# Kernel tuning notes

Hardware: AMD Instinct MI355X
Metric: run time of the kernel (lower is better)

Reference implementation:

```python
import jax, jax.numpy as jnp
import numpy as np

N = 100_000       # SUBJECT nodes
E = 1_000_000     # edges per relation
R = 3             # number of metapath relations
DIM_IN = 128
DIM_H = 128
HEADS = 8
D = DIM_H // HEADS   # per-head dim = 16
DIM_OUT = 4


def setup_inputs() -> dict:
    key = jax.random.key(0)
    ks = jax.random.split(key, 16)
    x = jax.random.normal(ks[0], (N, DIM_IN), dtype=jnp.float32)
    ei = [jax.random.randint(ks[1 + r], (2, E), 0, N, dtype=jnp.int32) for r in range(R)]
    s = 0.05
    return {
        "x": x,
        "edge_index_r0": ei[0],
        "edge_index_r1": ei[1],
        "edge_index_r2": ei[2],
        "proj_w": jax.random.normal(ks[4], (DIM_H, DIM_IN), dtype=jnp.float32) * s,
        "proj_b": jnp.zeros((DIM_H,), dtype=jnp.float32),
        "att_src": jax.random.normal(ks[5], (R, HEADS, D), dtype=jnp.float32) * s,
        "att_dst": jax.random.normal(ks[6], (R, HEADS, D), dtype=jnp.float32) * s,
        "k_w": jax.random.normal(ks[7], (DIM_H, DIM_H), dtype=jnp.float32) * s,
        "k_b": jnp.zeros((DIM_H,), dtype=jnp.float32),
        "q": jax.random.normal(ks[8], (DIM_H,), dtype=jnp.float32) * s,
        "lin_w": jax.random.normal(ks[9], (DIM_OUT, DIM_H), dtype=jnp.float32) * s,
        "lin_b": jnp.zeros((DIM_OUT,), dtype=jnp.float32),
    }


def _relation_out(h, a_src, a_dst, row, col, n):
    # GAT-style edge attention with softmax over destination neighborhoods.
    alpha = jax.nn.leaky_relu(a_src[row] + a_dst[col], 0.2)          # [E, H]
    m = jax.ops.segment_max(alpha, col, num_segments=n)              # [N, H]
    m = jax.lax.stop_gradient(jnp.where(jnp.isfinite(m), m, 0.0))
    e = jnp.exp(alpha - m[col])
    denom = jax.ops.segment_sum(e, col, num_segments=n)              # [N, H]
    alpha = e / (denom[col] + 1e-16)                                 # [E, H]
    msg = h[row] * alpha[..., None]                                  # [E, H, D]
    agg = jax.ops.segment_sum(msg, col, num_segments=n)              # [N, H, D]
    return jax.nn.relu(agg).reshape(n, HEADS * D)                    # [N, F]


def reference(x, edge_index_r0, edge_index_r1, edge_index_r2,
              proj_w, proj_b, att_src, att_dst, k_w, k_b, q, lin_w, lin_b):
    n = x.shape[0]
    h = (x @ proj_w.T + proj_b).reshape(n, HEADS, D)                 # node-type projection
    # per-node attention logits for every relation: [R, N, H]
    a_src = jnp.einsum('nhd,rhd->rnh', h, att_src)
    a_dst = jnp.einsum('nhd,rhd->rnh', h, att_dst)
    edge_indices = [edge_index_r0, edge_index_r1, edge_index_r2]
    outs = [_relation_out(h, a_src[r], a_dst[r], edge_indices[r][0], edge_indices[r][1], n)
            for r in range(R)]
    outs = jnp.stack(outs)                                           # [R, N, F]
    # semantic-level attention over metapaths
    score = jnp.einsum('f,rf->r', q, jnp.tanh(outs @ k_w.T + k_b).mean(axis=1))
    attn = jax.nn.softmax(score)                                     # [R]
    fused = jnp.einsum('r,rnf->nf', attn, outs)                      # [N, F]
    return fused @ lin_w.T + lin_b                                   # [N, DIM_OUT]
```

## Files before the change

kernel.cpp:

```cpp
#include <hip/hip_runtime.h>

#define N_NODES 100000
#define E_EDGES 1000000
#define R_REL   3
#define NBATCH  6250
#define NBLK    391
#define SEMBLK  782
#define CNT_BLKS  11721
#define PROJ_BLKS 391
#define A_BLKS    3125
#define BSUM_BLKS 1173
#define FILL_BLKS 3907
#define PULL_BLKS 3125

using bf16x8 = __attribute__((ext_vector_type(8))) short;
using f32x4  = __attribute__((ext_vector_type(4))) float;
using u32x2  = __attribute__((ext_vector_type(2))) unsigned int;

__device__ __forceinline__ float lrelu(float x) { return fmaxf(x, 0.2f * x); }

__device__ __forceinline__ short f2bf(float f) {
    unsigned u = __builtin_bit_cast(unsigned, f);
    u += 0x7FFFu + ((u >> 16) & 1u);
    return (short)(u >> 16);
}
__device__ __forceinline__ float bf_lo(unsigned u) {
    return __builtin_bit_cast(float, u << 16);
}
__device__ __forceinline__ float bf_hi(unsigned u) {
    return __builtin_bit_cast(float, u & 0xFFFF0000u);
}
__device__ __forceinline__ float bf2f(unsigned short u) {
    return __builtin_bit_cast(float, ((unsigned)u) << 16);
}

__global__ __launch_bounds__(256) void prep_kernel(
    const float* __restrict__ kw, const float* __restrict__ pw,
    const float* __restrict__ lw,
    short* __restrict__ kwB, short* __restrict__ pwB, short* __restrict__ linB)
{
    int idx = blockIdx.x * 256 + threadIdx.x;
    int which, rem;
    if      (idx < 16384) { which = 0; rem = idx; }
    else if (idx < 32768) { which = 1; rem = idx - 16384; }
    else if (idx < 34816) { which = 2; rem = idx - 32768; }
    else return;
    int e = rem & 7, lane = (rem >> 3) & 63, t = rem >> 9;
    int tj = (which == 2) ? 0 : (t >> 2);
    int tk = (which == 2) ? t : (t & 3);
    int j = tj * 16 + (lane & 15);
    int k = tk * 32 + (lane >> 4) * 8 + e;
    const float* src = (which == 0) ? kw : (which == 1) ? pw : lw;
    float v = (which == 2 && j >= 4) ? 0.f : src[j * 128 + k];
    short* dst = (which == 0) ? kwB : (which == 1) ? pwB : linB;
    dst[rem] = f2bf(v);
}

__device__ __forceinline__ void proj_body(
    int bx, const float* __restrict__ x, const short* __restrict__ pwB,
    const float* __restrict__ pb, unsigned short* __restrict__ h_bf)
{
    int wave = threadIdx.x >> 6, lane = threadIdx.x & 63;
    int row16 = lane & 15, kq = lane >> 4;
    for (int b = bx * 4 + wave; b < NBATCH; b += PROJ_BLKS * 4) {
        int nbase = b * 16;
        bf16x8 A[4];
        #pragma unroll
        for (int tk = 0; tk < 4; ++tk) {
            const float* px = x + (size_t)(nbase + row16) * 128 + tk * 32 + kq * 8;
            f32x4 lo = *(const f32x4*)px;
            f32x4 hi = *(const f32x4*)(px + 4);
            bf16x8 a;
            a[0] = f2bf(lo[0]); a[1] = f2bf(lo[1]); a[2] = f2bf(lo[2]); a[3] = f2bf(lo[3]);
            a[4] = f2bf(hi[0]); a[5] = f2bf(hi[1]); a[6] = f2bf(hi[2]); a[7] = f2bf(hi[3]);
            A[tk] = a;
        }
        #pragma unroll
        for (int tj = 0; tj < 8; ++tj) {
            f32x4 c = {0.f, 0.f, 0.f, 0.f};
            #pragma unroll
            for (int tk = 0; tk < 4; ++tk) {
                bf16x8 B = *(const bf16x8*)(pwB + ((size_t)(tj * 4 + tk) * 64 + lane) * 8);
                c = __builtin_amdgcn_mfma_f32_16x16x32_bf16(A[tk], B, c, 0, 0, 0);
            }
            int j = tj * 16 + row16;
            float bias = pb[j];
            #pragma unroll
            for (int m = 0; m < 4; ++m) {
                int n = nbase + kq * 4 + m;
                h_bf[(size_t)n * 128 + j] = (unsigned short)f2bf(c[m] + bias);
            }
        }
    }
}

__global__ __launch_bounds__(256) void count_proj_kernel(
    const int* __restrict__ e0, const int* __restrict__ e1, const int* __restrict__ e2,
    int* __restrict__ cnt, int* __restrict__ rank,
    const float* __restrict__ x, const short* __restrict__ pwB,
    const float* __restrict__ pb, unsigned short* __restrict__ h_bf)
{
    int b = blockIdx.x;
    if (b < CNT_BLKS) {
        int r = b / 3907, eb = b % 3907;
        const int* ei = (r == 0) ? e0 : (r == 1) ? e1 : e2;
        int e = eb * 256 + threadIdx.x;
        if (e < E_EDGES) {
            int k = atomicAdd(&cnt[r * N_NODES + ei[E_EDGES + e]], 1);
            rank[(size_t)r * E_EDGES + e] = k;
        }
    } else {
        proj_body(b - CNT_BLKS, x, pwB, pb, h_bf);
    }
}

__global__ __launch_bounds__(256) void a_bsum_kernel(
    const unsigned short* __restrict__ h_bf, const float* __restrict__ att_src,
    const float* __restrict__ att_dst,
    float* __restrict__ a_src, float* __restrict__ a_dst,
    const int* __restrict__ cnt, int* __restrict__ bsums)
{
    int b = blockIdx.x;
    if (b < A_BLKS) {
        int idx = b * 256 + threadIdx.x;
        if (idx >= N_NODES * 8) return;
        int n = idx >> 3, hd = idx & 7;
        float hv[16];
        const unsigned short* ph = h_bf + (size_t)n * 128 + hd * 16;
        #pragma unroll
        for (int d = 0; d < 16; ++d) hv[d] = bf2f(ph[d]);
        #pragma unroll
        for (int r = 0; r < 3; ++r) {
            float vs = 0.f, vd = 0.f;
            #pragma unroll
            for (int d = 0; d < 16; ++d) {
                vs += hv[d] * att_src[(r * 8 + hd) * 16 + d];
                vd += hv[d] * att_dst[(r * 8 + hd) * 16 + d];
            }
            a_src[((size_t)r * N_NODES + n) * 8 + hd] = vs;
            a_dst[((size_t)r * N_NODES + n) * 8 + hd] = vd;
        }
    } else {
        __shared__ int sh[256];
        int bb = b - A_BLKS;
        int r = bb / NBLK, blk = bb % NBLK, t = threadIdx.x;
        int i = blk * 256 + t;
        sh[t] = (i < N_NODES) ? cnt[r * N_NODES + i] : 0;
        __syncthreads();
        for (int d = 128; d > 0; d >>= 1) {
            if (t < d) sh[t] += sh[t + d];
            __syncthreads();
        }
        if (t == 0) bsums[r * NBLK + blk] = sh[0];
    }
}

__global__ __launch_bounds__(512) void bscan_kernel(
    const int* __restrict__ bsums, int* __restrict__ bpre)
{
    __shared__ int sh[512];
    int r = blockIdx.x, t = threadIdx.x;
    sh[t] = (t < NBLK) ? bsums[r * NBLK + t] : 0;
    __syncthreads();
    for (int d = 1; d < 512; d <<= 1) {
        int v = (t >= d) ? sh[t - d] : 0;
        __syncthreads();
        sh[t] += v;
        __syncthreads();
    }
    if (t < NBLK) bpre[r * NBLK + t] = (t > 0) ? sh[t - 1] : 0;
}

__global__ __launch_bounds__(256) void offwrite_kernel(
    const int* __restrict__ cnt, const int* __restrict__ bpre,
    int* __restrict__ off)
{
    __shared__ int sh[256];
    int r = blockIdx.y, b = blockIdx.x, t = threadIdx.x;
    int i = b * 256 + t;
    int c = (i < N_NODES) ? cnt[r * N_NODES + i] : 0;
    sh[t] = c;
    __syncthreads();
    for (int d = 1; d < 256; d <<= 1) {
        int v = (t >= d) ? sh[t - d] : 0;
        __syncthreads();
        sh[t] += v;
        __syncthreads();
    }
    if (i < N_NODES)
        off[r * N_NODES + i] = r * E_EDGES + bpre[r * NBLK + b] + (sh[t] - c);
}

__device__ __forceinline__ void fill_body(
    int r, int eb,
    const int* __restrict__ e0, const int* __restrict__ e1, const int* __restrict__ e2,
    const int* __restrict__ off, const int* __restrict__ rank,
    int* __restrict__ csr_rows)
{
    const int* ei = (r == 0) ? e0 : (r == 1) ? e1 : e2;
    int e = eb * 256 + threadIdx.x;
    if (e >= E_EDGES) return;
    int col = ei[E_EDGES + e];
    int pos = off[r * N_NODES + col] + rank[(size_t)r * E_EDGES + e];
    csr_rows[pos] = ei[e];
}

__global__ __launch_bounds__(256) void fill_kernel(
    const int* __restrict__ e0, const int* __restrict__ e1, const int* __restrict__ e2,
    const int* __restrict__ off, const int* __restrict__ rank,
    int* __restrict__ csr_rows, int r)
{
    fill_body(r, blockIdx.x, e0, e1, e2, off, rank, csr_rows);
}

__device__ __forceinline__ void pull_body(
    int bx, int r,
    const unsigned short* __restrict__ h_bf, const float* __restrict__ a_src,
    const float* __restrict__ a_dst, const int* __restrict__ cnt,
    const int* __restrict__ off, const int* __restrict__ csr_rows,
    unsigned int* __restrict__ outs_bf)
{
    int tid = threadIdx.x;
    int wave = tid >> 6, lane = tid & 63;
    int half = lane >> 5, hl = lane & 31;
    int hd = hl >> 2;
    const size_t rbase = (size_t)r * N_NODES;
    const int CSR_LAST = R_REL * E_EDGES - 1;

    int nb = (bx * 8 + wave * 2 + half) * 4;

    int deg4[4], dm1[4], st4[4];
    float adv[4];
    int kmax = 0;
    #pragma unroll
    for (int i = 0; i < 4; ++i) {
        size_t rn = rbase + (nb + i);
        deg4[i] = cnt[rn];
        st4[i]  = off[rn];
        dm1[i]  = max(deg4[i] - 1, 0);
        adv[i]  = a_dst[rn * 8 + hd];
        kmax = max(kmax, deg4[i]);
    }
    float acc[4][4] = {};
    float den[4] = {0.f, 0.f, 0.f, 0.f};

    for (int k = 0; k < kmax; k += 2) {
        int rowA[4], rowB[4];
        #pragma unroll
        for (int i = 0; i < 4; ++i) {
            int kA = min(k, dm1[i]), kB = min(k + 1, dm1[i]);
            rowA[i] = csr_rows[min(st4[i] + kA, CSR_LAST)];
            rowB[i] = csr_rows[min(st4[i] + kB, CSR_LAST)];
        }
        float aA[4], aB[4];
        u32x2 hA[4], hB[4];
        #pragma unroll
        for (int i = 0; i < 4; ++i) {
            aA[i] = a_src[(rbase + rowA[i]) * 8 + hd];
            aB[i] = a_src[(rbase + rowB[i]) * 8 + hd];
            hA[i] = *(const u32x2*)(h_bf + (size_t)rowA[i] * 128 + 4 * hl);
            hB[i] = *(const u32x2*)(h_bf + (size_t)rowB[i] * 128 + 4 * hl);
        }
        #pragma unroll
        for (int i = 0; i < 4; ++i) {
            float eA = __expf(lrelu(aA[i] + adv[i]));
            float eB = __expf(lrelu(aB[i] + adv[i]));
            eA = (k     < deg4[i]) ? eA : 0.f;
            eB = (k + 1 < deg4[i]) ? eB : 0.f;
            acc[i][0] += eA * bf_lo(hA[i][0]);
            acc[i][1] += eA * bf_hi(hA[i][0]);
            acc[i][2] += eA * bf_lo(hA[i][1]);
            acc[i][3] += eA * bf_hi(hA[i][1]);
            den[i]    += eA;
            acc[i][0] += eB * bf_lo(hB[i][0]);
            acc[i][1] += eB * bf_hi(hB[i][0]);
            acc[i][2] += eB * bf_lo(hB[i][1]);
            acc[i][3] += eB * bf_hi(hB[i][1]);
            den[i]    += eB;
        }
    }
    #pragma unroll
    for (int i = 0; i < 4; ++i) {
        float inv = 1.f / (den[i] + 1e-16f);
        float o0 = fmaxf(acc[i][0] * inv, 0.f);
        float o1 = fmaxf(acc[i][1] * inv, 0.f);
        float o2 = fmaxf(acc[i][2] * inv, 0.f);
        float o3 = fmaxf(acc[i][3] * inv, 0.f);
        u32x2 p;
        p[0] = (unsigned)(unsigned short)f2bf(o0) | ((unsigned)(unsigned short)f2bf(o1) << 16);
        p[1] = (unsigned)(unsigned short)f2bf(o2) | ((unsigned)(unsigned short)f2bf(o3) << 16);
        *(u32x2*)(outs_bf + (size_t)(nb + i) * 64 + 2 * hl) = p;
    }
}

__global__ __launch_bounds__(256) void pull_kernel(
    const unsigned short* __restrict__ h_bf, const float* __restrict__ a_src,
    const float* __restrict__ a_dst, const int* __restrict__ cnt,
    const int* __restrict__ off, const int* __restrict__ csr_rows,
    unsigned int* __restrict__ outs_bf, int r)
{
    pull_body(blockIdx.x, r, h_bf, a_src, a_dst, cnt, off, csr_rows, outs_bf);
}

__global__ __launch_bounds__(256) void pull0_fill12_kernel(
    const unsigned short* __restrict__ h_bf, const float* __restrict__ a_src,
    const float* __restrict__ a_dst, const int* __restrict__ cnt,
    const int* __restrict__ off, const int* __restrict__ csr_rows,
    unsigned int* __restrict__ outs_bf,
    const int* __restrict__ e0, const int* __restrict__ e1, const int* __restrict__ e2,
    const int* __restrict__ rank, int* __restrict__ csr_w)
{
    int b = blockIdx.x;
    if (b < PULL_BLKS) {
        pull_body(b, 0, h_bf, a_src, a_dst, cnt, off, csr_rows, outs_bf);
    } else {
        int bb = b - PULL_BLKS;
        int r = 1 + bb / FILL_BLKS, eb = bb % FILL_BLKS;
        fill_body(r, eb, e0, e1, e2, off, rank, csr_w);
    }
}

__global__ __launch_bounds__(256) void semantic_kernel(
    const unsigned short* __restrict__ outs_bf,
    const short* __restrict__ kwB, const short* __restrict__ linB,
    const float* __restrict__ kb,
    float* __restrict__ proj_out, float* __restrict__ redpart, int r)
{
    __shared__ float sh[4][128];
    int wave = threadIdx.x >> 6, lane = threadIdx.x & 63;
    int row16 = lane & 15, kq = lane >> 4;
    const size_t rbase = (size_t)r * N_NODES;

    float kbv[8];
    #pragma unroll
    for (int tj = 0; tj < 8; ++tj) kbv[tj] = kb[tj * 16 + row16];
    float red_acc[8] = {0.f,0.f,0.f,0.f,0.f,0.f,0.f,0.f};

    for (int b = blockIdx.x * 4 + wave; b < NBATCH; b += gridDim.x * 4) {
        int nbase = b * 16;
        bf16x8 A[4];
        #pragma unroll
        for (int tk = 0; tk < 4; ++tk)
            A[tk] = *(const bf16x8*)(outs_bf + (size_t)(nbase + row16) * 128 + tk * 32 + kq * 8);

        #pragma unroll
        for (int tj = 0; tj < 8; ++tj) {
            f32x4 c = {0.f, 0.f, 0.f, 0.f};
            #pragma unroll
            for (int tk = 0; tk < 4; ++tk) {
                bf16x8 B = *(const bf16x8*)(kwB + ((size_t)(tj * 4 + tk) * 64 + lane) * 8);
                c = __builtin_amdgcn_mfma_f32_16x16x32_bf16(A[tk], B, c, 0, 0, 0);
            }
            float ts = 0.f;
            #pragma unroll
            for (int m = 0; m < 4; ++m) {
                float s = c[m] + kbv[tj];
                float ex = __expf(2.f * s);
                ts += 1.f - 2.f / (ex + 1.f);
            }
            red_acc[tj] += ts;
        }
        {
            f32x4 c = {0.f, 0.f, 0.f, 0.f};
            #pragma unroll
            for (int tk = 0; tk < 4; ++tk) {
                bf16x8 B = *(const bf16x8*)(linB + ((size_t)tk * 64 + lane) * 8);
                c = __builtin_amdgcn_mfma_f32_16x16x32_bf16(A[tk], B, c, 0, 0, 0);
            }
            if (row16 < 4) {
                #pragma unroll
                for (int m = 0; m < 4; ++m) {
                    int n = nbase + kq * 4 + m;
                    proj_out[(rbase + n) * 4 + row16] = c[m];
                }
            }
        }
    }

    #pragma unroll
    for (int tj = 0; tj < 8; ++tj) {
        float v = red_acc[tj];
        v += __shfl_xor(v, 16);
        v += __shfl_xor(v, 32);
        if (lane < 16) sh[wave][tj * 16 + lane] = v;
    }
    __syncthreads();
    int t = threadIdx.x;
    if (t < 128) {
        float p = sh[0][t] + sh[1][t] + sh[2][t] + sh[3][t];
        redpart[((size_t)r * SEMBLK + blockIdx.x) * 128 + t] = p;
    }
}

__global__ __launch_bounds__(256) void redreduce_kernel(
    const float* __restrict__ redpart, float* __restrict__ red)
{
    __shared__ float sh[2][128];
    int r = blockIdx.x;
    int t = threadIdx.x;
    int j = t & 127, half = t >> 7;
    float s = 0.f;
    for (int b = half; b < SEMBLK; b += 2)
        s += redpart[((size_t)r * SEMBLK + b) * 128 + j];
    sh[half][j] = s;
    __syncthreads();
    if (t < 128) red[r * 128 + t] = sh[0][t] + sh[1][t];
}

__global__ void attn_kernel(const float* __restrict__ red, const float* __restrict__ q,
                            float* __restrict__ attn)
{
    int lane = threadIdx.x;
    float p[3];
    #pragma unroll
    for (int r = 0; r < 3; ++r) {
        float v = q[lane] * red[r * 128 + lane] + q[lane + 64] * red[r * 128 + lane + 64];
        for (int sft = 32; sft; sft >>= 1) v += __shfl_down(v, sft);
        p[r] = v;
    }
    if (lane == 0) {
        float s0 = p[0] / (float)N_NODES;
        float s1 = p[1] / (float)N_NODES;
        float s2 = p[2] / (float)N_NODES;
        float m = fmaxf(s0, fmaxf(s1, s2));
        float e0 = __expf(s0 - m), e1 = __expf(s1 - m), e2 = __expf(s2 - m);
        float inv = 1.f / (e0 + e1 + e2);
        attn[0] = e0 * inv; attn[1] = e1 * inv; attn[2] = e2 * inv;
    }
}

__global__ __launch_bounds__(256) void final_kernel(
    const float* __restrict__ proj_out, const float* __restrict__ attn,
    const float* __restrict__ lb, float* __restrict__ out)
{
    int i = blockIdx.x * 256 + threadIdx.x;
    if (i >= N_NODES * 4) return;
    int o = i & 3;
    out[i] = attn[0] * proj_out[i]
           + attn[1] * proj_out[(size_t)N_NODES * 4 + i]
           + attn[2] * proj_out[(size_t)2 * N_NODES * 4 + i]
           + lb[o];
}

extern "C" void kernel_launch(void* const* d_in, const int* in_sizes, int n_in,
                              void* d_out, int out_size, void* d_ws, size_t ws_size,
                              hipStream_t stream)
{
    const float* x       = (const float*)d_in[0];
    const int*   e0      = (const int*)d_in[1];
    const int*   e1      = (const int*)d_in[2];
    const int*   e2      = (const int*)d_in[3];
    const float* pw      = (const float*)d_in[4];
    const float* pb      = (const float*)d_in[5];
    const float* att_src = (const float*)d_in[6];
    const float* att_dst = (const float*)d_in[7];
    const float* kw      = (const float*)d_in[8];
    const float* kb      = (const float*)d_in[9];
    const float* q       = (const float*)d_in[10];
    const float* lw      = (const float*)d_in[11];
    const float* lb      = (const float*)d_in[12];
    float* out = (float*)d_out;

    float* ws = (float*)d_ws;
    unsigned short* h_bf    = (unsigned short*)ws;
    float*          a_src   = ws + 6400000;
    float*          a_dst   = ws + 8800000;
    unsigned int*   outs_bf = (unsigned int*)(ws + 11200000);
    float*          proj_out= ws + 17600000;
    float*          red     = ws + 18800000;
    float*          attn    = ws + 18800384;
    short*          kwB     = (short*)(ws + 18800388);
    short*          pwB     = (short*)(ws + 18808580);
    short*          linB    = (short*)(ws + 18816772);
    int*            cnt     = (int*)(ws + 18817796);
    int*            off     = (int*)(ws + 19117796);
    int*            csr_rows= (int*)(ws + 19417796);
    int*            bsums   = (int*)(ws + 22417796);
    int*            bpre    = (int*)(ws + 22418969);
    float*          redpart = ws + 22420224;

    const size_t BIG_NEED = (size_t)(22720512 + 3000000) * 4;
    bool big = ws_size >= BIG_NEED;
    int* rank = big ? (int*)(ws + 22720512)
                    : (int*)outs_bf;

    hipMemsetAsync(cnt, 0, 300000 * sizeof(int), stream);

    prep_kernel<<<dim3(136), dim3(256), 0, stream>>>(kw, pw, lw, kwB, pwB, linB);
    count_proj_kernel<<<dim3(CNT_BLKS + PROJ_BLKS), dim3(256), 0, stream>>>(
        e0, e1, e2, cnt, rank, x, pwB, pb, h_bf);
    a_bsum_kernel<<<dim3(A_BLKS + BSUM_BLKS), dim3(256), 0, stream>>>(
        h_bf, att_src, att_dst, a_src, a_dst, cnt, bsums);
    bscan_kernel<<<dim3(3), dim3(512), 0, stream>>>(bsums, bpre);
    offwrite_kernel<<<dim3(NBLK, 3), dim3(256), 0, stream>>>(cnt, bpre, off);

    if (big) {
        fill_kernel<<<dim3(FILL_BLKS), dim3(256), 0, stream>>>(
            e0, e1, e2, off, rank, csr_rows, 0);
        pull0_fill12_kernel<<<dim3(PULL_BLKS + 2 * FILL_BLKS), dim3(256), 0, stream>>>(
            h_bf, a_src, a_dst, cnt, off, csr_rows, outs_bf,
            e0, e1, e2, rank, csr_rows);
        semantic_kernel<<<dim3(SEMBLK), dim3(256), 0, stream>>>(
            (const unsigned short*)outs_bf, kwB, linB, kb, proj_out, redpart, 0);
        for (int r = 1; r < 3; ++r) {
            pull_kernel<<<dim3(PULL_BLKS), dim3(256), 0, stream>>>(
                h_bf, a_src, a_dst, cnt, off, csr_rows, outs_bf, r);
            semantic_kernel<<<dim3(SEMBLK), dim3(256), 0, stream>>>(
                (const unsigned short*)outs_bf, kwB, linB, kb, proj_out, redpart, r);
        }
    } else {
        for (int r = 0; r < 3; ++r)
            fill_kernel<<<dim3(FILL_BLKS), dim3(256), 0, stream>>>(
                e0, e1, e2, off, rank, csr_rows, r);
        for (int r = 0; r < 3; ++r) {
            pull_kernel<<<dim3(PULL_BLKS), dim3(256), 0, stream>>>(
                h_bf, a_src, a_dst, cnt, off, csr_rows, outs_bf, r);
            semantic_kernel<<<dim3(SEMBLK), dim3(256), 0, stream>>>(
                (const unsigned short*)outs_bf, kwB, linB, kb, proj_out, redpart, r);
        }
    }

    redreduce_kernel<<<dim3(3), dim3(256), 0, stream>>>(redpart, red);
    attn_kernel<<<dim3(1), dim3(64), 0, stream>>>(red, q, attn);
    final_kernel<<<dim3(1563), dim3(256), 0, stream>>>(proj_out, attn, lb, out);
}
```

Measured before the change: 532.0 us.

## Double-buffer relation outputs and co-schedule pull with semantic, move attention logits into fill

Adds a second bf16 output buffer so the pull for relation r+1 and the semantic projection for relation r run in one fused launch. The per-node attention logit computation moves out of the bsum kernel and into the fill kernel for relation 0, and bsum becomes a standalone 2D-grid kernel. It also sets unroll 1 on the MFMA tj loops and adds occupancy hints of 6 blocks to reduce register pressure. The aim is to overlap the gather-bound pull with the MFMA-bound semantic work and cut launch boundaries, at the cost of more workspace and a path that only activates when the larger workspace is available.

Result: slower. 567.9 us (+6.7%).

```diff
diff --git a/kernel.cpp b/kernel.cpp
--- a/kernel.cpp
+++ b/kernel.cpp
@@ -9,7 +9,6 @@
 #define CNT_BLKS  11721
 #define PROJ_BLKS 391
 #define A_BLKS    3125
-#define BSUM_BLKS 1173
 #define FILL_BLKS 3907
 #define PULL_BLKS 3125
 
@@ -75,7 +74,7 @@
             a[4] = f2bf(hi[0]); a[5] = f2bf(hi[1]); a[6] = f2bf(hi[2]); a[7] = f2bf(hi[3]);
             A[tk] = a;
         }
-        #pragma unroll
+        #pragma unroll 1
         for (int tj = 0; tj < 8; ++tj) {
             f32x4 c = {0.f, 0.f, 0.f, 0.f};
             #pragma unroll
@@ -94,7 +93,7 @@
     }
 }
 
-__global__ __launch_bounds__(256) void count_proj_kernel(
+__global__ __launch_bounds__(256, 6) void count_proj_kernel(
     const int* __restrict__ e0, const int* __restrict__ e1, const int* __restrict__ e2,
     int* __restrict__ cnt, int* __restrict__ rank,
     const float* __restrict__ x, const short* __restrict__ pwB,
@@ -114,45 +113,19 @@
     }
 }
 
-__global__ __launch_bounds__(256) void a_bsum_kernel(
-    const unsigned short* __restrict__ h_bf, const float* __restrict__ att_src,
-    const float* __restrict__ att_dst,
-    float* __restrict__ a_src, float* __restrict__ a_dst,
+__global__ __launch_bounds__(256) void bsum_kernel(
     const int* __restrict__ cnt, int* __restrict__ bsums)
 {
-    int b = blockIdx.x;
-    if (b < A_BLKS) {
-        int idx = b * 256 + threadIdx.x;
-        if (idx >= N_NODES * 8) return;
-        int n = idx >> 3, hd = idx & 7;
-        float hv[16];
-        const unsigned short* ph = h_bf + (size_t)n * 128 + hd * 16;
-        #pragma unroll
-        for (int d = 0; d < 16; ++d) hv[d] = bf2f(ph[d]);
-        #pragma unroll
-        for (int r = 0; r < 3; ++r) {
-            float vs = 0.f, vd = 0.f;
-            #pragma unroll
-            for (int d = 0; d < 16; ++d) {
-                vs += hv[d] * att_src[(r * 8 + hd) * 16 + d];
-                vd += hv[d] * att_dst[(r * 8 + hd) * 16 + d];
-            }
-            a_src[((size_t)r * N_NODES + n) * 8 + hd] = vs;
-            a_dst[((size_t)r * N_NODES + n) * 8 + hd] = vd;
-        }
-    } else {
-        __shared__ int sh[256];
-        int bb = b - A_BLKS;
-        int r = bb / NBLK, blk = bb % NBLK, t = threadIdx.x;
-        int i = blk * 256 + t;
-        sh[t] = (i < N_NODES) ? cnt[r * N_NODES + i] : 0;
+    __shared__ int sh[256];
+    int r = blockIdx.y, b = blockIdx.x, t = threadIdx.x;
+    int i = b * 256 + t;
+    sh[t] = (i < N_NODES) ? cnt[r * N_NODES + i] : 0;
+    __syncthreads();
+    for (int d = 128; d > 0; d >>= 1) {
+        if (t < d) sh[t] += sh[t + d];
         __syncthreads();
-        for (int d = 128; d > 0; d >>= 1) {
-            if (t < d) sh[t] += sh[t + d];
-            __syncthreads();
-        }
-        if (t == 0) bsums[r * NBLK + blk] = sh[0];
-    }
+    }
+    if (t == 0) bsums[r * NBLK + b] = sh[0];
 }
 
 __global__ __launch_bounds__(512) void bscan_kernel(
@@ -191,6 +164,31 @@
         off[r * N_NODES + i] = r * E_EDGES + bpre[r * NBLK + b] + (sh[t] - c);
 }
 
+__device__ __forceinline__ void a_body(
+    int bx, const unsigned short* __restrict__ h_bf,
+    const float* __restrict__ att_src, const float* __restrict__ att_dst,
+    float* __restrict__ a_src, float* __restrict__ a_dst)
+{
+    int idx = bx * 256 + threadIdx.x;
+    if (idx >= N_NODES * 8) return;
+    int n = idx >> 3, hd = idx & 7;
+    float hv[16];
+    const unsigned short* ph = h_bf + (size_t)n * 128 + hd * 16;
+    #pragma unroll
+    for (int d = 0; d < 16; ++d) hv[d] = bf2f(ph[d]);
+    #pragma unroll
+    for (int r = 0; r < 3; ++r) {
+        float vs = 0.f, vd = 0.f;
+        #pragma unroll
+        for (int d = 0; d < 16; ++d) {
+            vs += hv[d] * att_src[(r * 8 + hd) * 16 + d];
+            vd += hv[d] * att_dst[(r * 8 + hd) * 16 + d];
+        }
+        a_src[((size_t)r * N_NODES + n) * 8 + hd] = vs;
+        a_dst[((size_t)r * N_NODES + n) * 8 + hd] = vd;
+    }
+}
+
 __device__ __forceinline__ void fill_body(
     int r, int eb,
     const int* __restrict__ e0, const int* __restrict__ e1, const int* __restrict__ e2,
@@ -205,12 +203,21 @@
     csr_rows[pos] = ei[e];
 }
 
-__global__ __launch_bounds__(256) void fill_kernel(
+__global__ __launch_bounds__(256) void a_fill_kernel(
+    const unsigned short* __restrict__ h_bf, const float* __restrict__ att_src,
+    const float* __restrict__ att_dst, float* __restrict__ a_src,
+    float* __restrict__ a_dst,
     const int* __restrict__ e0, const int* __restrict__ e1, const int* __restrict__ e2,
     const int* __restrict__ off, const int* __restrict__ rank,
-    int* __restrict__ csr_rows, int r)
-{
-    fill_body(r, blockIdx.x, e0, e1, e2, off, rank, csr_rows);
+    int* __restrict__ csr_rows)
+{
+    int b = blockIdx.x;
+    if (b < A_BLKS) {
+        a_body(b, h_bf, att_src, att_dst, a_src, a_dst);
+    } else {
+        int bb = b - A_BLKS;
+        fill_body(bb / FILL_BLKS, bb % FILL_BLKS, e0, e1, e2, off, rank, csr_rows);
+    }
 }
 
 __device__ __forceinline__ void pull_body(
@@ -293,35 +300,8 @@
     }
 }
 
-__global__ __launch_bounds__(256) void pull_kernel(
-    const unsigned short* __restrict__ h_bf, const float* __restrict__ a_src,
-    const float* __restrict__ a_dst, const int* __restrict__ cnt,
-    const int* __restrict__ off, const int* __restrict__ csr_rows,
-    unsigned int* __restrict__ outs_bf, int r)
-{
-    pull_body(blockIdx.x, r, h_bf, a_src, a_dst, cnt, off, csr_rows, outs_bf);
-}
-
-__global__ __launch_bounds__(256) void pull0_fill12_kernel(
-    const unsigned short* __restrict__ h_bf, const float* __restrict__ a_src,
-    const float* __restrict__ a_dst, const int* __restrict__ cnt,
-    const int* __restrict__ off, const int* __restrict__ csr_rows,
-    unsigned int* __restrict__ outs_bf,
-    const int* __restrict__ e0, const int* __restrict__ e1, const int* __restrict__ e2,
-    const int* __restrict__ rank, int* __restrict__ csr_w)
-{
-    int b = blockIdx.x;
-    if (b < PULL_BLKS) {
-        pull_body(b, 0, h_bf, a_src, a_dst, cnt, off, csr_rows, outs_bf);
-    } else {
-        int bb = b - PULL_BLKS;
-        int r = 1 + bb / FILL_BLKS, eb = bb % FILL_BLKS;
-        fill_body(r, eb, e0, e1, e2, off, rank, csr_w);
-    }
-}
-
-__global__ __launch_bounds__(256) void semantic_kernel(
-    const unsigned short* __restrict__ outs_bf,
+__device__ __forceinline__ void semantic_body(
+    int bx, const unsigned short* __restrict__ outs_bf,
     const short* __restrict__ kwB, const short* __restrict__ linB,
     const float* __restrict__ kb,
     float* __restrict__ proj_out, float* __restrict__ redpart, int r)
@@ -336,14 +316,14 @@
     for (int tj = 0; tj < 8; ++tj) kbv[tj] = kb[tj * 16 + row16];
     float red_acc[8] = {0.f,0.f,0.f,0.f,0.f,0.f,0.f,0.f};
 
-    for (int b = blockIdx.x * 4 + wave; b < NBATCH; b += gridDim.x * 4) {
+    for (int b = bx * 4 + wave; b < NBATCH; b += SEMBLK * 4) {
         int nbase = b * 16;
         bf16x8 A[4];
         #pragma unroll
         for (int tk = 0; tk < 4; ++tk)
             A[tk] = *(const bf16x8*)(outs_bf + (size_t)(nbase + row16) * 128 + tk * 32 + kq * 8);
 
-        #pragma unroll
+        #pragma unroll 1
         for (int tj = 0; tj < 8; ++tj) {
             f32x4 c = {0.f, 0.f, 0.f, 0.f};
             #pragma unroll
@@ -388,7 +368,59 @@
     int t = threadIdx.x;
     if (t < 128) {
         float p = sh[0][t] + sh[1][t] + sh[2][t] + sh[3][t];
-        redpart[((size_t)r * SEMBLK + blockIdx.x) * 128 + t] = p;
+        redpart[((size_t)r * SEMBLK + bx) * 128 + t] = p;
+    }
+}
+
+__global__ __launch_bounds__(256) void pull_kernel(
+    const unsigned short* __restrict__ h_bf, const float* __restrict__ a_src,
+    const float* __restrict__ a_dst, const int* __restrict__ cnt,
+    const int* __restrict__ off, const int* __restrict__ csr_rows,
+    unsigned int* __restrict__ outs_bf, int r)
+{
+    pull_body(blockIdx.x, r, h_bf, a_src, a_dst, cnt, off, csr_rows, outs_bf);
+}
+
+__global__ __launch_bounds__(256) void semantic_kernel(
+    const unsigned short* __restrict__ outs_bf,
+    const short* __restrict__ kwB, const short* __restrict__ linB,
+    const float* __restrict__ kb,
+    float* __restrict__ proj_out, float* __restrict__ redpart, int r)
+{
+    semantic_body(blockIdx.x, outs_bf, kwB, linB, kb, proj_out, redpart, r);
+}
+
+__global__ __launch_bounds__(256) void pull0_fill12_kernel(
+    const unsigned short* __restrict__ h_bf, const float* __restrict__ a_src,
+    const float* __restrict__ a_dst, const int* __restrict__ cnt,
+    const int* __restrict__ off, const int* __restrict__ csr_rows,
+    unsigned int* __restrict__ outs_bf,
+    const int* __restrict__ e0, const int* __restrict__ e1, const int* __restrict__ e2,
+    const int* __restrict__ rank, int* __restrict__ csr_w)
+{
+    int b = blockIdx.x;
+    if (b < PULL_BLKS) {
+        pull_body(b, 0, h_bf, a_src, a_dst, cnt, off, csr_rows, outs_bf);
+    } else {
+        int bb = b - PULL_BLKS;
+        fill_body(1 + bb / FILL_BLKS, bb % FILL_BLKS, e0, e1, e2, off, rank, csr_w);
+    }
+}
+
+__global__ __launch_bounds__(256, 6) void pull_sem_kernel(
+    const unsigned short* __restrict__ h_bf, const float* __restrict__ a_src,
+    const float* __restrict__ a_dst, const int* __restrict__ cnt,
+    const int* __restrict__ off, const int* __restrict__ csr_rows,
+    unsigned int* __restrict__ outsW, const unsigned short* __restrict__ outsR,
+    const short* __restrict__ kwB, const short* __restrict__ linB,
+    const float* __restrict__ kb, float* __restrict__ proj_out,
+    float* __restrict__ redpart, int rpull, int rsem)
+{
+    int b = blockIdx.x;
+    if (b < PULL_BLKS) {
+        pull_body(b, rpull, h_bf, a_src, a_dst, cnt, off, csr_rows, outsW);
+    } else {
+        semantic_body(b - PULL_BLKS, outsR, kwB, linB, kb, proj_out, redpart, rsem);
     }
 }
 
@@ -465,7 +497,7 @@
     unsigned short* h_bf    = (unsigned short*)ws;
     float*          a_src   = ws + 6400000;
     float*          a_dst   = ws + 8800000;
-    unsigned int*   outs_bf = (unsigned int*)(ws + 11200000);
+    unsigned int*   outs0   = (unsigned int*)(ws + 11200000);
     float*          proj_out= ws + 17600000;
     float*          red     = ws + 18800000;
     float*          attn    = ws + 18800384;
@@ -479,44 +511,58 @@
     int*            bpre    = (int*)(ws + 22418969);
     float*          redpart = ws + 22420224;
 
-    const size_t BIG_NEED = (size_t)(22720512 + 3000000) * 4;
-    bool big = ws_size >= BIG_NEED;
-    int* rank = big ? (int*)(ws + 22720512)
-                    : (int*)outs_bf;
+    const size_t P1_NEED = (size_t)(22720512 + 3000000) * 4;
+    const size_t P2_NEED = (size_t)(22720512 + 3000000 + 6400000) * 4;
+    bool p2 = ws_size >= P2_NEED;
+    bool p1 = ws_size >= P1_NEED;
+    int* rank = p1 ? (int*)(ws + 22720512) : (int*)outs0;
+    unsigned int* outs1 = p2 ? (unsigned int*)(ws + 25720512) : outs0;
 
     hipMemsetAsync(cnt, 0, 300000 * sizeof(int), stream);
 
     prep_kernel<<<dim3(136), dim3(256), 0, stream>>>(kw, pw, lw, kwB, pwB, linB);
     count_proj_kernel<<<dim3(CNT_BLKS + PROJ_BLKS), dim3(256), 0, stream>>>(
         e0, e1, e2, cnt, rank, x, pwB, pb, h_bf);
-    a_bsum_kernel<<<dim3(A_BLKS + BSUM_BLKS), dim3(256), 0, stream>>>(
-        h_bf, att_src, att_dst, a_src, a_dst, cnt, bsums);
+    bsum_kernel<<<dim3(NBLK, 3), dim3(256), 0, stream>>>(cnt, bsums);
     bscan_kernel<<<dim3(3), dim3(512), 0, stream>>>(bsums, bpre);
     offwrite_kernel<<<dim3(NBLK, 3), dim3(256), 0, stream>>>(cnt, bpre, off);
 
-    if (big) {
-        fill_kernel<<<dim3(FILL_BLKS), dim3(256), 0, stream>>>(
-            e0, e1, e2, off, rank, csr_rows, 0);
+    if (p2) {
+        a_fill_kernel<<<dim3(A_BLKS + FILL_BLKS), dim3(256), 0, stream>>>(
+            h_bf, att_src, att_dst, a_src, a_dst, e0, e1, e2, off, rank, csr_rows);
         pull0_fill12_kernel<<<dim3(PULL_BLKS + 2 * FILL_BLKS), dim3(256), 0, stream>>>(
-            h_bf, a_src, a_dst, cnt, off, csr_rows, outs_bf,
+            h_bf, a_src, a_dst, cnt, off, csr_rows, outs0,
+            e0, e1, e2, rank, csr_rows);
+        pull_sem_kernel<<<dim3(PULL_BLKS + SEMBLK), dim3(256), 0, stream>>>(
+            h_bf, a_src, a_dst, cnt, off, csr_rows, outs1,
+            (const unsigned short*)outs0, kwB, linB, kb, proj_out, redpart, 1, 0);
+        pull_sem_kernel<<<dim3(PULL_BLKS + SEMBLK), dim3(256), 0, stream>>>(
+            h_bf, a_src, a_dst, cnt, off, csr_rows, outs0,
+            (const unsigned short*)outs1, kwB, linB, kb, proj_out, redpart, 2, 1);
+        semantic_kernel<<<dim3(SEMBLK), dim3(256), 0, stream>>>(
+            (const unsigned short*)outs0, kwB, linB, kb, proj_out, redpart, 2);
+    } else if (p1) {
+        a_fill_kernel<<<dim3(A_BLKS + FILL_BLKS), dim3(256), 0, stream>>>(
+            h_bf, att_src, att_dst, a_src, a_dst, e0, e1, e2, off, rank, csr_rows);
+        pull0_fill12_kernel<<<dim3(PULL_BLKS + 2 * FILL_BLKS), dim3(256), 0, stream>>>(
+            h_bf, a_src, a_dst, cnt, off, csr_rows, outs0,
             e0, e1, e2, rank, csr_rows);
         semantic_kernel<<<dim3(SEMBLK), dim3(256), 0, stream>>>(
-            (const unsigned short*)outs_bf, kwB, linB, kb, proj_out, redpart, 0);
+            (const unsigned short*)outs0, kwB, linB, kb, proj_out, redpart, 0);
         for (int r = 1; r < 3; ++r) {
             pull_kernel<<<dim3(PULL_BLKS), dim3(256), 0, stream>>>(
-                h_bf, a_src, a_dst, cnt, off, csr_rows, outs_bf, r);
+                h_bf, a_src, a_dst, cnt, off, csr_rows, outs0, r);
             semantic_kernel<<<dim3(SEMBLK), dim3(256), 0, stream>>>(
-                (const unsigned short*)outs_bf, kwB, linB, kb, proj_out, redpart, r);
+                (const unsigned short*)outs0, kwB, linB, kb, proj_out, redpart, r);
         }
     } else {
-        for (int r = 0; r < 3; ++r)
-            fill_kernel<<<dim3(FILL_BLKS), dim3(256), 0, stream>>>(
-                e0, e1, e2, off, rank, csr_rows, r);
+        a_fill_kernel<<<dim3(A_BLKS + 3 * FILL_BLKS), dim3(256), 0, stream>>>(
+            h_bf, att_src, att_dst, a_src, a_dst, e0, e1, e2, off, rank, csr_rows);
         for (int r = 0; r < 3; ++r) {
             pull_kernel<<<dim3(PULL_BLKS), dim3(256), 0, stream>>>(
-                h_bf, a_src, a_dst, cnt, off, csr_rows, outs_bf, r);
+                h_bf, a_src, a_dst, cnt, off, csr_rows, outs0, r);
             semantic_kernel<<<dim3(SEMBLK), dim3(256), 0, stream>>>(
-                (const unsigned short*)outs_bf, kwB, linB, kb, proj_out, redpart, r);
+                (const unsigned short*)outs0, kwB, linB, kb, proj_out, redpart, r);
         }
     }
 
```

## Fuse semantic attention into pull kernel via LDS and regroup kernel launches

Applied to the files above, without the earlier changes.

The per-relation aggregation kernel now writes its bf16 outputs to shared memory and immediately runs the key-projection MFMA, tanh-sum and output projection within the same block, eliminating the global outs buffer and separate semantic kernels. The attention-logit computation moves from the bsum kernel into a combined kernel with relation-0 CSR fill, and the workspace is rearranged so rank always has its own region. This removes global round trips and several launches but increases per-block redpart partials (3125 per relation) that the reduce kernel must sum, and adds syncthreads to the pull path.

Measured after the change: 772.0 us. +45.1%, slower.

```diff
diff --git a/kernel.cpp b/kernel.cpp
--- a/kernel.cpp
+++ b/kernel.cpp
@@ -5,13 +5,12 @@
 #define R_REL   3
 #define NBATCH  6250
 #define NBLK    391
-#define SEMBLK  782
 #define CNT_BLKS  11721
 #define PROJ_BLKS 391
 #define A_BLKS    3125
-#define BSUM_BLKS 1173
 #define FILL_BLKS 3907
-#define PULL_BLKS 3125
+#define PS_BLKS   3125
+#define REDN      3125
 
 using bf16x8 = __attribute__((ext_vector_type(8))) short;
 using f32x4  = __attribute__((ext_vector_type(4))) float;
@@ -114,45 +113,19 @@
     }
 }
 
-__global__ __launch_bounds__(256) void a_bsum_kernel(
-    const unsigned short* __restrict__ h_bf, const float* __restrict__ att_src,
-    const float* __restrict__ att_dst,
-    float* __restrict__ a_src, float* __restrict__ a_dst,
+__global__ __launch_bounds__(256) void bsum_kernel(
     const int* __restrict__ cnt, int* __restrict__ bsums)
 {
-    int b = blockIdx.x;
-    if (b < A_BLKS) {
-        int idx = b * 256 + threadIdx.x;
-        if (idx >= N_NODES * 8) return;
-        int n = idx >> 3, hd = idx & 7;
-        float hv[16];
-        const unsigned short* ph = h_bf + (size_t)n * 128 + hd * 16;
-        #pragma unroll
-        for (int d = 0; d < 16; ++d) hv[d] = bf2f(ph[d]);
-        #pragma unroll
-        for (int r = 0; r < 3; ++r) {
-            float vs = 0.f, vd = 0.f;
-            #pragma unroll
-            for (int d = 0; d < 16; ++d) {
-                vs += hv[d] * att_src[(r * 8 + hd) * 16 + d];
-                vd += hv[d] * att_dst[(r * 8 + hd) * 16 + d];
-            }
-            a_src[((size_t)r * N_NODES + n) * 8 + hd] = vs;
-            a_dst[((size_t)r * N_NODES + n) * 8 + hd] = vd;
-        }
-    } else {
-        __shared__ int sh[256];
-        int bb = b - A_BLKS;
-        int r = bb / NBLK, blk = bb % NBLK, t = threadIdx.x;
-        int i = blk * 256 + t;
-        sh[t] = (i < N_NODES) ? cnt[r * N_NODES + i] : 0;
+    __shared__ int sh[256];
+    int r = blockIdx.y, b = blockIdx.x, t = threadIdx.x;
+    int i = b * 256 + t;
+    sh[t] = (i < N_NODES) ? cnt[r * N_NODES + i] : 0;
+    __syncthreads();
+    for (int d = 128; d > 0; d >>= 1) {
+        if (t < d) sh[t] += sh[t + d];
         __syncthreads();
-        for (int d = 128; d > 0; d >>= 1) {
-            if (t < d) sh[t] += sh[t + d];
-            __syncthreads();
-        }
-        if (t == 0) bsums[r * NBLK + blk] = sh[0];
-    }
+    }
+    if (t == 0) bsums[r * NBLK + b] = sh[0];
 }
 
 __global__ __launch_bounds__(512) void bscan_kernel(
@@ -191,6 +164,31 @@
         off[r * N_NODES + i] = r * E_EDGES + bpre[r * NBLK + b] + (sh[t] - c);
 }
 
+__device__ __forceinline__ void a_body(
+    int bx, const unsigned short* __restrict__ h_bf,
+    const float* __restrict__ att_src, const float* __restrict__ att_dst,
+    float* __restrict__ a_src, float* __restrict__ a_dst)
+{
+    int idx = bx * 256 + threadIdx.x;
+    if (idx >= N_NODES * 8) return;
+    int n = idx >> 3, hd = idx & 7;
+    float hv[16];
+    const unsigned short* ph = h_bf + (size_t)n * 128 + hd * 16;
+    #pragma unroll
+    for (int d = 0; d < 16; ++d) hv[d] = bf2f(ph[d]);
+    #pragma unroll
+    for (int r = 0; r < 3; ++r) {
+        float vs = 0.f, vd = 0.f;
+        #pragma unroll
+        for (int d = 0; d < 16; ++d) {
+            vs += hv[d] * att_src[(r * 8 + hd) * 16 + d];
+            vd += hv[d] * att_dst[(r * 8 + hd) * 16 + d];
+        }
+        a_src[((size_t)r * N_NODES + n) * 8 + hd] = vs;
+        a_dst[((size_t)r * N_NODES + n) * 8 + hd] = vd;
+    }
+}
+
 __device__ __forceinline__ void fill_body(
     int r, int eb,
     const int* __restrict__ e0, const int* __restrict__ e1, const int* __restrict__ e2,
@@ -205,20 +203,32 @@
     csr_rows[pos] = ei[e];
 }
 
-__global__ __launch_bounds__(256) void fill_kernel(
+__global__ __launch_bounds__(256) void a_fill_kernel(
+    const unsigned short* __restrict__ h_bf, const float* __restrict__ att_src,
+    const float* __restrict__ att_dst, float* __restrict__ a_src,
+    float* __restrict__ a_dst,
     const int* __restrict__ e0, const int* __restrict__ e1, const int* __restrict__ e2,
     const int* __restrict__ off, const int* __restrict__ rank,
-    int* __restrict__ csr_rows, int r)
-{
-    fill_body(r, blockIdx.x, e0, e1, e2, off, rank, csr_rows);
-}
-
-__device__ __forceinline__ void pull_body(
+    int* __restrict__ csr_rows)
+{
+    int b = blockIdx.x;
+    if (b < A_BLKS) {
+        a_body(b, h_bf, att_src, att_dst, a_src, a_dst);
+    } else {
+        int bb = b - A_BLKS;
+        fill_body(bb / FILL_BLKS, bb % FILL_BLKS, e0, e1, e2, off, rank, csr_rows);
+    }
+}
+
+__device__ __forceinline__ void pullsem_body(
     int bx, int r,
     const unsigned short* __restrict__ h_bf, const float* __restrict__ a_src,
     const float* __restrict__ a_dst, const int* __restrict__ cnt,
     const int* __restrict__ off, const int* __restrict__ csr_rows,
-    unsigned int* __restrict__ outs_bf)
+    const short* __restrict__ kwB, const short* __restrict__ linB,
+    const float* __restrict__ kb,
+    float* __restrict__ proj_out, float* __restrict__ redpart,
+    unsigned int* lds_out, float (*sh)[128])
 {
     int tid = threadIdx.x;
     int wave = tid >> 6, lane = tid & 63;
@@ -227,7 +237,8 @@
     const size_t rbase = (size_t)r * N_NODES;
     const int CSR_LAST = R_REL * E_EDGES - 1;
 
-    int nb = (bx * 8 + wave * 2 + half) * 4;
+    int unit = wave * 2 + half;
+    int nb = (bx * 8 + unit) * 4;
 
     int deg4[4], dm1[4], st4[4];
     float adv[4];
@@ -289,106 +300,95 @@
         u32x2 p;
         p[0] = (unsigned)(unsigned short)f2bf(o0) | ((unsigned)(unsigned short)f2bf(o1) << 16);
         p[1] = (unsigned)(unsigned short)f2bf(o2) | ((unsigned)(unsigned short)f2bf(o3) << 16);
-        *(u32x2*)(outs_bf + (size_t)(nb + i) * 64 + 2 * hl) = p;
-    }
-}
-
-__global__ __launch_bounds__(256) void pull_kernel(
+        int rl = unit * 4 + i;
+        *(u32x2*)&lds_out[rl * 68 + 2 * hl] = p;
+    }
+    __syncthreads();
+
+    int batch = wave & 1;
+    int tjlo = (wave >> 1) * 4;
+    int row16 = lane & 15, kq = lane >> 4;
+    bf16x8 A[4];
+    const char* abase = (const char*)lds_out + (batch * 16 + row16) * 272 + kq * 16;
+    #pragma unroll
+    for (int tk = 0; tk < 4; ++tk)
+        A[tk] = *(const bf16x8*)(abase + tk * 64);
+
+    #pragma unroll
+    for (int t = 0; t < 4; ++t) {
+        int tj = tjlo + t;
+        f32x4 c = {0.f, 0.f, 0.f, 0.f};
+        #pragma unroll
+        for (int tk = 0; tk < 4; ++tk) {
+            bf16x8 B = *(const bf16x8*)(kwB + ((size_t)(tj * 4 + tk) * 64 + lane) * 8);
+            c = __builtin_amdgcn_mfma_f32_16x16x32_bf16(A[tk], B, c, 0, 0, 0);
+        }
+        float kbv = kb[tj * 16 + row16];
+        float ts = 0.f;
+        #pragma unroll
+        for (int m = 0; m < 4; ++m) {
+            float s = c[m] + kbv;
+            float ex = __expf(2.f * s);
+            ts += 1.f - 2.f / (ex + 1.f);
+        }
+        ts += __shfl_xor(ts, 16);
+        ts += __shfl_xor(ts, 32);
+        if (lane < 16) sh[batch][tj * 16 + lane] = ts;
+    }
+    if (wave < 2) {
+        f32x4 c = {0.f, 0.f, 0.f, 0.f};
+        #pragma unroll
+        for (int tk = 0; tk < 4; ++tk) {
+            bf16x8 B = *(const bf16x8*)(linB + ((size_t)tk * 64 + lane) * 8);
+            c = __builtin_amdgcn_mfma_f32_16x16x32_bf16(A[tk], B, c, 0, 0, 0);
+        }
+        if (row16 < 4) {
+            #pragma unroll
+            for (int m = 0; m < 4; ++m) {
+                int n = bx * 32 + batch * 16 + kq * 4 + m;
+                proj_out[(rbase + n) * 4 + row16] = c[m];
+            }
+        }
+    }
+    __syncthreads();
+    int t = threadIdx.x;
+    if (t < 128)
+        redpart[((size_t)r * REDN + bx) * 128 + t] = sh[0][t] + sh[1][t];
+}
+
+__global__ __launch_bounds__(256) void pullsem_kernel(
     const unsigned short* __restrict__ h_bf, const float* __restrict__ a_src,
     const float* __restrict__ a_dst, const int* __restrict__ cnt,
     const int* __restrict__ off, const int* __restrict__ csr_rows,
-    unsigned int* __restrict__ outs_bf, int r)
-{
-    pull_body(blockIdx.x, r, h_bf, a_src, a_dst, cnt, off, csr_rows, outs_bf);
-}
-
-__global__ __launch_bounds__(256) void pull0_fill12_kernel(
+    const short* __restrict__ kwB, const short* __restrict__ linB,
+    const float* __restrict__ kb,
+    float* __restrict__ proj_out, float* __restrict__ redpart, int r)
+{
+    __shared__ __align__(16) unsigned int lds_out[32 * 68];
+    __shared__ float sh[2][128];
+    pullsem_body(blockIdx.x, r, h_bf, a_src, a_dst, cnt, off, csr_rows,
+                 kwB, linB, kb, proj_out, redpart, lds_out, sh);
+}
+
+__global__ __launch_bounds__(256) void ps0_fill12_kernel(
     const unsigned short* __restrict__ h_bf, const float* __restrict__ a_src,
     const float* __restrict__ a_dst, const int* __restrict__ cnt,
     const int* __restrict__ off, const int* __restrict__ csr_rows,
-    unsigned int* __restrict__ outs_bf,
+    const short* __restrict__ kwB, const short* __restrict__ linB,
+    const float* __restrict__ kb,
+    float* __restrict__ proj_out, float* __restrict__ redpart,
     const int* __restrict__ e0, const int* __restrict__ e1, const int* __restrict__ e2,
     const int* __restrict__ rank, int* __restrict__ csr_w)
 {
+    __shared__ __align__(16) unsigned int lds_out[32 * 68];
+    __shared__ float sh[2][128];
     int b = blockIdx.x;
-    if (b < PULL_BLKS) {
-        pull_body(b, 0, h_bf, a_src, a_dst, cnt, off, csr_rows, outs_bf);
+    if (b < PS_BLKS) {
+        pullsem_body(b, 0, h_bf, a_src, a_dst, cnt, off, csr_rows,
+                     kwB, linB, kb, proj_out, redpart, lds_out, sh);
     } else {
-        int bb = b - PULL_BLKS;
-        int r = 1 + bb / FILL_BLKS, eb = bb % FILL_BLKS;
-        fill_body(r, eb, e0, e1, e2, off, rank, csr_w);
-    }
-}
-
-__global__ __launch_bounds__(256) void semantic_kernel(
-    const unsigned short* __restrict__ outs_bf,
-    const short* __restrict__ kwB, const short* __restrict__ linB,
-    const float* __restrict__ kb,
-    float* __restrict__ proj_out, float* __restrict__ redpart, int r)
-{
-    __shared__ float sh[4][128];
-    int wave = threadIdx.x >> 6, lane = threadIdx.x & 63;
-    int row16 = lane & 15, kq = lane >> 4;
-    const size_t rbase = (size_t)r * N_NODES;
-
-    float kbv[8];
-    #pragma unroll
-    for (int tj = 0; tj < 8; ++tj) kbv[tj] = kb[tj * 16 + row16];
-    float red_acc[8] = {0.f,0.f,0.f,0.f,0.f,0.f,0.f,0.f};
-
-    for (int b = blockIdx.x * 4 + wave; b < NBATCH; b += gridDim.x * 4) {
-        int nbase = b * 16;
-        bf16x8 A[4];
-        #pragma unroll
-        for (int tk = 0; tk < 4; ++tk)
-            A[tk] = *(const bf16x8*)(outs_bf + (size_t)(nbase + row16) * 128 + tk * 32 + kq * 8);
-
-        #pragma unroll
-        for (int tj = 0; tj < 8; ++tj) {
-            f32x4 c = {0.f, 0.f, 0.f, 0.f};
-            #pragma unroll
-            for (int tk = 0; tk < 4; ++tk) {
-                bf16x8 B = *(const bf16x8*)(kwB + ((size_t)(tj * 4 + tk) * 64 + lane) * 8);
-                c = __builtin_amdgcn_mfma_f32_16x16x32_bf16(A[tk], B, c, 0, 0, 0);
-            }
-            float ts = 0.f;
-            #pragma unroll
-            for (int m = 0; m < 4; ++m) {
-                float s = c[m] + kbv[tj];
-                float ex = __expf(2.f * s);
-                ts += 1.f - 2.f / (ex + 1.f);
-            }
-            red_acc[tj] += ts;
-        }
-        {
-            f32x4 c = {0.f, 0.f, 0.f, 0.f};
-            #pragma unroll
-            for (int tk = 0; tk < 4; ++tk) {
-                bf16x8 B = *(const bf16x8*)(linB + ((size_t)tk * 64 + lane) * 8);
-                c = __builtin_amdgcn_mfma_f32_16x16x32_bf16(A[tk], B, c, 0, 0, 0);
-            }
-            if (row16 < 4) {
-                #pragma unroll
-                for (int m = 0; m < 4; ++m) {
-                    int n = nbase + kq * 4 + m;
-                    proj_out[(rbase + n) * 4 + row16] = c[m];
-                }
-            }
-        }
-    }
-
-    #pragma unroll
-    for (int tj = 0; tj < 8; ++tj) {
-        float v = red_acc[tj];
-        v += __shfl_xor(v, 16);
-        v += __shfl_xor(v, 32);
-        if (lane < 16) sh[wave][tj * 16 + lane] = v;
-    }
-    __syncthreads();
-    int t = threadIdx.x;
-    if (t < 128) {
-        float p = sh[0][t] + sh[1][t] + sh[2][t] + sh[3][t];
-        redpart[((size_t)r * SEMBLK + blockIdx.x) * 128 + t] = p;
+        int bb = b - PS_BLKS;
+        fill_body(1 + bb / FILL_BLKS, bb % FILL_BLKS, e0, e1, e2, off, rank, csr_w);
     }
 }
 
@@ -400,8 +400,8 @@
     int t = threadIdx.x;
     int j = t & 127, half = t >> 7;
     float s = 0.f;
-    for (int b = half; b < SEMBLK; b += 2)
-        s += redpart[((size_t)r * SEMBLK + b) * 128 + j];
+    for (int b = half; b < REDN; b += 2)
+        s += redpart[((size_t)r * REDN + b) * 128 + j];
     sh[half][j] = s;
     __syncthreads();
     if (t < 128) red[r * 128 + t] = sh[0][t] + sh[1][t];
@@ -465,7 +465,8 @@
     unsigned short* h_bf    = (unsigned short*)ws;
     float*          a_src   = ws + 6400000;
     float*          a_dst   = ws + 8800000;
-    unsigned int*   outs_bf = (unsigned int*)(ws + 11200000);
+    int*            rank    = (int*)(ws + 11200000);
+    float*          redpart = ws + 14200000;
     float*          proj_out= ws + 17600000;
     float*          red     = ws + 18800000;
     float*          attn    = ws + 18800384;
@@ -477,48 +478,27 @@
     int*            csr_rows= (int*)(ws + 19417796);
     int*            bsums   = (int*)(ws + 22417796);
     int*            bpre    = (int*)(ws + 22418969);
-    float*          redpart = ws + 22420224;
-
-    const size_t BIG_NEED = (size_t)(22720512 + 3000000) * 4;
-    bool big = ws_size >= BIG_NEED;
-    int* rank = big ? (int*)(ws + 22720512)
-                    : (int*)outs_bf;
 
     hipMemsetAsync(cnt, 0, 300000 * sizeof(int), stream);
 
     prep_kernel<<<dim3(136), dim3(256), 0, stream>>>(kw, pw, lw, kwB, pwB, linB);
     count_proj_kernel<<<dim3(CNT_BLKS + PROJ_BLKS), dim3(256), 0, stream>>>(
         e0, e1, e2, cnt, rank, x, pwB, pb, h_bf);
-    a_bsum_kernel<<<dim3(A_BLKS + BSUM_BLKS), dim3(256), 0, stream>>>(
-        h_bf, att_src, att_dst, a_src, a_dst, cnt, bsums);
+    bsum_kernel<<<dim3(NBLK, 3), dim3(256), 0, stream>>>(cnt, bsums);
     bscan_kernel<<<dim3(3), dim3(512), 0, stream>>>(bsums, bpre);
     offwrite_kernel<<<dim3(NBLK, 3), dim3(256), 0, stream>>>(cnt, bpre, off);
 
-    if (big) {
-        fill_kernel<<<dim3(FILL_BLKS), dim3(256), 0, stream>>>(
-            e0, e1, e2, off, rank, csr_rows, 0);
-        pull0_fill12_kernel<<<dim3(PULL_BLKS + 2 * FILL_BLKS), dim3(256), 0, stream>>>(
-            h_bf, a_src, a_dst, cnt, off, csr_rows, outs_bf,
-            e0, e1, e2, rank, csr_rows);
-        semantic_kernel<<<dim3(SEMBLK), dim3(256), 0, stream>>>(
-            (const unsigned short*)outs_bf, kwB, linB, kb, proj_out, redpart, 0);
-        for (int r = 1; r < 3; ++r) {
-            pull_kernel<<<dim3(PULL_BLKS), dim3(256), 0, stream>>>(
-                h_bf, a_src, a_dst, cnt, off, csr_rows, outs_bf, r);
-            semantic_kernel<<<dim3(SEMBLK), dim3(256), 0, stream>>>(
-                (const unsigned short*)outs_bf, kwB, linB, kb, proj_out, redpart, r);
-        }
-    } else {
-        for (int r = 0; r < 3; ++r)
-            fill_kernel<<<dim3(FILL_BLKS), dim3(256), 0, stream>>>(
-                e0, e1, e2, off, rank, csr_rows, r);
-        for (int r = 0; r < 3; ++r) {
-            pull_kernel<<<dim3(PULL_BLKS), dim3(256), 0, stream>>>(
-                h_bf, a_src, a_dst, cnt, off, csr_rows, outs_bf, r);
-            semantic_kernel<<<dim3(SEMBLK), dim3(256), 0, stream>>>(
-                (const unsigned short*)outs_bf, kwB, linB, kb, proj_out, redpart, r);
-        }
-    }
+    a_fill_kernel<<<dim3(A_BLKS + FILL_BLKS), dim3(256), 0, stream>>>(
+        h_bf, att_src, att_dst, a_src, a_dst, e0, e1, e2, off, rank, csr_rows);
+    ps0_fill12_kernel<<<dim3(PS_BLKS + 2 * FILL_BLKS), dim3(256), 0, stream>>>(
+        h_bf, a_src, a_dst, cnt, off, csr_rows, kwB, linB, kb,
+        proj_out, redpart, e0, e1, e2, rank, csr_rows);
+    pullsem_kernel<<<dim3(PS_BLKS), dim3(256), 0, stream>>>(
+        h_bf, a_src, a_dst, cnt, off, csr_rows, kwB, linB, kb,
+        proj_out, redpart, 1);
+    pullsem_kernel<<<dim3(PS_BLKS), dim3(256), 0, stream>>>(
+        h_bf, a_src, a_dst, cnt, off, csr_rows, kwB, linB, kb,
+        proj_out, redpart, 2);
 
     redreduce_kernel<<<dim3(3), dim3(256), 0, stream>>>(redpart, red);
     attn_kernel<<<dim3(1), dim3(64), 0, stream>>>(red, q, attn);
```
